# Kernel tuning notes

Hardware: AMD Instinct MI355X
Metric: run time of the kernel (lower is better)

The kernel has to match this reference:

```python
import jax, jax.numpy as jnp
import numpy as np

N_NODES = 50000
N_EDGES = 400000
N_GRAPHS = 512
F = 32        # num_features
NB = 32       # mp_num_basis_fn
ZMAX = 118
CUTOFF = 5.0
NSPH = 9      # (mp_max_degree+1)^2 with max_degree=2
DEG_IDX = jnp.array([0, 1, 1, 1, 2, 2, 2, 2, 2])  # degree of each spherical component


def _bernstein(u, n=NB):
    # reciprocal_bernstein radial basis: Bernstein polynomials of degree n-1 at u in [0,1)
    k = jnp.arange(n, dtype=jnp.float32)
    log_binom = (jax.scipy.special.gammaln(float(n)) - jax.scipy.special.gammaln(k + 1.0)
                 - jax.scipy.special.gammaln(float(n) - k))
    u = jnp.clip(u, 1e-7, 1.0 - 1e-7)[..., None]
    return jnp.exp(log_binom + k * jnp.log(u) + (float(n) - 1.0 - k) * jnp.log1p(-u))


def _smooth_cutoff(r, cutoff=CUTOFF):
    t = r / cutoff
    return jnp.where(t < 1.0, jnp.exp(1.0 - 1.0 / jnp.clip(1.0 - t * t, 1e-7, None)), 0.0)


def _sph(u):
    # real spherical harmonics (cartesian normalization) up to degree 2; u: (E,3) unit vectors
    x, y, z = u[:, 0], u[:, 1], u[:, 2]
    c = jnp.sqrt(jnp.float32(3.0))
    return jnp.stack([jnp.ones_like(x), y, z, x,
                      c * x * y, c * y * z, 0.5 * (3.0 * z * z - 1.0),
                      c * z * x, 0.5 * c * (x * x - y * y)], axis=-1)


def _dense(x, W, b):
    # equivariant Dense: shared kernel over spherical components, bias only on scalar (l=0)
    y = jnp.einsum('nmf,fg->nmg', x, W)
    return y.at[:, 0, :].add(b)


def _silu_gate(x):
    # equivariant silu: scalar channel gates all degrees (scalar part -> exact silu)
    return x * jax.nn.sigmoid(x[:, 0:1, :])


def setup_inputs() -> dict:
    key = jax.random.key(0)
    ks = jax.random.split(key, 24)
    s = 1.0 / np.sqrt(F)
    sb = 1.0 / np.sqrt(NB)
    inp = {
        'positions': 2.0 * jax.random.normal(ks[0], (N_NODES, 3), jnp.float32),
        'embed': jax.random.normal(ks[1], (ZMAX, F), jnp.float32),
        'Wy0': sb * jax.random.normal(ks[2], (3, NB, F), jnp.float32),
        'Wx0': sb * jax.random.normal(ks[3], (3, NB, F), jnp.float32),
        'W1_0': s * jax.random.normal(ks[4], (F, F), jnp.float32),
        'b1_0': jnp.zeros((F,), jnp.float32),
        'W2_0': s * jax.random.normal(ks[5], (F, F), jnp.float32),
        'b2_0': jnp.zeros((F,), jnp.float32),
        'c0': jnp.full((1,), 0.5, jnp.float32),
        'Wr_last': sb * jax.random.normal(ks[6], (NB, F), jnp.float32),
        'W1_1': s * jax.random.normal(ks[7], (F, F), jnp.float32),
        'b1_1': jnp.zeros((F,), jnp.float32),
        'W2_1': s * jax.random.normal(ks[8], (F, F), jnp.float32),
        'b2_1': jnp.zeros((F,), jnp.float32),
        'c1': jnp.full((1,), 0.5, jnp.float32),
        'Wro1': s * jax.random.normal(ks[9], (F, F), jnp.float32),
        'bro1': jnp.zeros((F,), jnp.float32),
        'Wro2': s * jax.random.normal(ks[10], (F, 1), jnp.float32),
        'bro2': jnp.zeros((1,), jnp.float32),
        'atomic_bias': jax.random.normal(ks[11], (ZMAX,), jnp.float32),
        'atomic_numbers': jax.random.randint(ks[12], (N_NODES,), 0, ZMAX, jnp.int32),
        'dst_idx': jax.random.randint(ks[13], (N_EDGES,), 0, N_NODES, jnp.int32),
        'src_idx': jax.random.randint(ks[14], (N_EDGES,), 0, N_NODES, jnp.int32),
        'batch_segments': jnp.sort(jax.random.randint(ks[15], (N_NODES,), 0, N_GRAPHS, jnp.int32)),
        'graph_mask': jnp.ones((N_GRAPHS,), jnp.bool_),
    }
    return inp


def reference(positions, embed, Wy0, Wx0, W1_0, b1_0, W2_0, b2_0, c0,
              Wr_last, W1_1, b1_1, W2_1, b2_1, c1,
              Wro1, bro1, Wro2, bro2, atomic_bias,
              atomic_numbers, dst_idx, src_idx, batch_segments, graph_mask):
    # --- edge geometry (gather_src/gather_dst) ---
    disp = positions[src_idx] - positions[dst_idx]                # (E,3)
    r = jnp.sqrt(jnp.sum(disp * disp, axis=-1) + 1e-12)           # (E,)
    u = disp / r[:, None]
    Y = _sph(u)                                                   # (E,9)
    rbf = _bernstein(r / (r + 1.0)) * _smooth_cutoff(r)[:, None]  # (E,NB)

    # --- atomic embedding, lifted to (N, 9, F) with zero higher degrees ---
    x0 = embed[atomic_numbers]                                    # (N,F)
    x = jnp.concatenate([x0[:, None, :], jnp.zeros((N_NODES, NSPH - 1, F), x0.dtype)], axis=1)

    # --- iteration 0: full-degree equivariant message pass ---
    wy = jnp.einsum('eb,lbf->elf', rbf, Wy0)[:, DEG_IDX, :]       # (E,9,F) radial weights, (0,l)->l path
    wx = jnp.einsum('eb,lbf->elf', rbf, Wx0)[:, DEG_IDX, :]       # (l,0)->l path
    xs = x[src_idx]                                               # (E,9,F)
    msg = wy * Y[:, :, None] * xs[:, 0:1, :] + wx * xs
    y = jax.ops.segment_sum(msg, dst_idx, num_segments=N_NODES)   # (N,9,F)
    y = x + y
    y = _silu_gate(_dense(y, W1_0, b1_0))
    y = _dense(y, W2_0, b2_0)
    x = x + jax.nn.silu(c0) * y                                   # y_nl == 0 (era disabled)

    # --- iteration 1 (last): max_degree=0 message pass, then reduce to scalars ---
    w0 = rbf @ Wr_last                                            # (E,F)
    msg0 = w0 * x[src_idx, 0, :]
    y0 = jax.ops.segment_sum(msg0, dst_idx, num_segments=N_NODES) # (N,F)
    xs0 = x[:, 0, :]                                              # change_max_degree -> scalars
    y0 = xs0 + y0
    y0 = jax.nn.silu(y0 @ W1_1 + b1_1)
    y0 = y0 @ W2_1 + b2_1
    xs0 = xs0 + jax.nn.silu(c1) * y0

    # --- atomic readout and per-graph sum ---
    h = jax.nn.silu(xs0 @ Wro1 + bro1)
    e_atom = (h @ Wro2)[:, 0] + bro2[0] + atomic_bias[atomic_numbers]
    e_graph = jax.ops.segment_sum(e_atom, batch_segments, num_segments=N_GRAPHS)
    return jnp.where(graph_mask, e_graph, 0.0)
```

## Files before the change

kernel.cpp:

```cpp
#include <hip/hip_runtime.h>
#include <math.h>

#define NNODES 50000
#define NEDGES 400000
#define NGRAPHS 512
#define FDIM 32
#define CAP 32

#define NHALVES 4096
#define NQ   (NNODES / NHALVES)
#define NREM (NNODES % NHALVES)

static constexpr float BINOM31[32] = {
    1.f, 31.f, 465.f, 4495.f, 31465.f, 169911.f, 736281.f, 2629575.f,
    7888725.f, 20160075.f, 44352165.f, 84672315.f, 141120525.f, 206253075.f,
    265182525.f, 300540195.f, 300540195.f, 265182525.f, 206253075.f,
    141120525.f, 84672315.f, 44352165.f, 20160075.f, 7888725.f, 2629575.f,
    736281.f, 169911.f, 31465.f, 4495.f, 465.f, 31.f, 1.f
};

__device__ __forceinline__ float fast_rcp(float x) {
    return __builtin_amdgcn_rcpf(x);
}
__device__ __forceinline__ float silu(float x) {
    return x * fast_rcp(1.0f + __expf(-x));
}

__global__ __launch_bounds__(256) void build_csr(
    const float* __restrict__ pos,
    const int* __restrict__ srci, const int* __restrict__ dsti,
    const int* __restrict__ Z,
    float4* __restrict__ pay, int* __restrict__ deg)
{
    int e = blockIdx.x * 256 + threadIdx.x;
    if (e >= NEDGES) return;
    int s = srci[e], d = dsti[e];
    float dx = pos[3 * s]     - pos[3 * d];
    float dy = pos[3 * s + 1] - pos[3 * d + 1];
    float dz = pos[3 * s + 2] - pos[3 * d + 2];
    float r = sqrtf(dx * dx + dy * dy + dz * dz + 1e-12f);
    if (r >= 5.0f) return;

    float t = r * 0.2f;
    float q = fmaxf(1.0f - t * t, 1e-7f);
    float cut = __expf(1.0f - fast_rcp(q));
    float v = fast_rcp(r + 1.0f);
    float v2 = v * v, v4 = v2 * v2, v8 = v4 * v4, v16 = v8 * v8;
    float scale = v16 * v8 * v4 * v2 * v * cut;

    int rank = atomicAdd(&deg[d], 1);
    if (rank < CAP)
        pay[(size_t)d * CAP + rank] =
            make_float4(r, scale,
                        __int_as_float(s * FDIM),
                        __int_as_float(Z[s] * FDIM));
}

#define GATHER8(ACC, XSRC, SEL)                                            \
    float ACC = 0.0f;                                                      \
    for (int j = 0; j < dgc; j += 8) {                                     \
        float rr[8], sc[8], xg[8], hh[8];                                  \
        _Pragma("unroll")                                                  \
        for (int k = 0; k < 8; ++k) {                                      \
            float4 _p = pl[j + k];                                         \
            rr[k] = _p.x; sc[k] = _p.y;                                    \
            xg[k] = (XSRC)[__float_as_int(_p.SEL) + f];                    \
        }                                                                  \
        _Pragma("unroll")                                                  \
        for (int k = 0; k < 8; ++k) hh[k] = cw[31];                        \
        _Pragma("unroll")                                                  \
        for (int t = 30; t >= 0; --t) {                                    \
            _Pragma("unroll")                                              \
            for (int k = 0; k < 8; ++k)                                    \
                hh[k] = fmaf(hh[k], rr[k], cw[t]);                         \
        }                                                                  \
        _Pragma("unroll")                                                  \
        for (int k = 0; k < 8; ++k)                                        \
            ACC = fmaf(sc[k] * hh[k], xg[k], ACC);                         \
    }

#define MATVEC32R(RES, WR, BIAS) do {                                      \
    float4 _q0=yp[0], _q1=yp[1], _q2=yp[2], _q3=yp[3];                     \
    float4 _q4=yp[4], _q5=yp[5], _q6=yp[6], _q7=yp[7];                     \
    float _a0=(BIAS), _a1=0.f, _a2=0.f, _a3=0.f;                           \
    _a0=fmaf(_q0.x,WR[ 0],_a0); _a0=fmaf(_q0.y,WR[ 1],_a0);                \
    _a0=fmaf(_q0.z,WR[ 2],_a0); _a0=fmaf(_q0.w,WR[ 3],_a0);                \
    _a1=fmaf(_q1.x,WR[ 4],_a1); _a1=fmaf(_q1.y,WR[ 5],_a1);                \
    _a1=fmaf(_q1.z,WR[ 6],_a1); _a1=fmaf(_q1.w,WR[ 7],_a1);                \
    _a2=fmaf(_q2.x,WR[ 8],_a2); _a2=fmaf(_q2.y,WR[ 9],_a2);                \
    _a2=fmaf(_q2.z,WR[10],_a2); _a2=fmaf(_q2.w,WR[11],_a2);                \
    _a3=fmaf(_q3.x,WR[12],_a3); _a3=fmaf(_q3.y,WR[13],_a3);                \
    _a3=fmaf(_q3.z,WR[14],_a3); _a3=fmaf(_q3.w,WR[15],_a3);                \
    _a0=fmaf(_q4.x,WR[16],_a0); _a0=fmaf(_q4.y,WR[17],_a0);                \
    _a0=fmaf(_q4.z,WR[18],_a0); _a0=fmaf(_q4.w,WR[19],_a0);                \
    _a1=fmaf(_q5.x,WR[20],_a1); _a1=fmaf(_q5.y,WR[21],_a1);                \
    _a1=fmaf(_q5.z,WR[22],_a1); _a1=fmaf(_q5.w,WR[23],_a1);                \
    _a2=fmaf(_q6.x,WR[24],_a2); _a2=fmaf(_q6.y,WR[25],_a2);                \
    _a2=fmaf(_q6.z,WR[26],_a2); _a2=fmaf(_q6.w,WR[27],_a2);                \
    _a3=fmaf(_q7.x,WR[28],_a3); _a3=fmaf(_q7.y,WR[29],_a3);                \
    _a3=fmaf(_q7.z,WR[30],_a3); _a3=fmaf(_q7.w,WR[31],_a3);                \
    RES = (_a0+_a1)+(_a2+_a3); } while (0)

__device__ __forceinline__ void half_range(int h, int& n0, int& n1) {
    int a = h < NREM ? h * (NQ + 1) : NREM * (NQ + 1) + (h - NREM) * NQ;
    n0 = a;
    n1 = a + (h < NREM ? NQ + 1 : NQ);
}

__global__ __launch_bounds__(256, 2) void fused_a(
    const float4* __restrict__ pay, const int* __restrict__ deg,
    const float* __restrict__ embed, const int* __restrict__ Z,
    const float* __restrict__ Wy0, const float* __restrict__ Wx0,
    const float* __restrict__ W1, const float* __restrict__ b1,
    const float* __restrict__ W2, const float* __restrict__ b2,
    const float* __restrict__ c0,
    float* __restrict__ x1buf)
{
    __shared__ __align__(16) float ylds[4][64];
    __shared__ __align__(16) float4 plds[4][2][CAP];
    int tid = threadIdx.x;
    int widx = tid >> 6;
    int lane = tid & 63;
    int f    = lane & 31;
    int half = lane >> 5;

    float cw[32], w1r[32], w2r[32];
    #pragma unroll
    for (int k = 0; k < 32; ++k) {
        cw[k]  = BINOM31[k] * (Wy0[k * FDIM + f] + Wx0[k * FDIM + f]);
        w1r[k] = W1[k * FDIM + f];
        w2r[k] = W2[k * FDIM + f];
    }
    float b1f = b1[f], b2f = b2[f];
    float sc0 = silu(c0[0]);

    int hidx = (blockIdx.x * 4 + widx) * 2 + half;
    int n0, n1;
    half_range(hidx, n0, n1);

    float* yrow = &ylds[widx][half * 32];
    const float4* yp = (const float4*)yrow;
    float4* pl = &plds[widx][half][0];

    int dgc = min(deg[n0], CAP);
    float4 pv0 = make_float4(0.f, 0.f, 0.f, 0.f);
    if (f < dgc) pv0 = pay[(size_t)n0 * CAP + f];
    int zc = Z[n0];
    pl[f] = pv0;
    float x0 = embed[zc * FDIM + f];

    for (int n = n0; n < n1; ++n) {
        int nn = (n + 1 < n1) ? n + 1 : n;
        int dgn = min(deg[nn], CAP);
        int zn  = Z[nn];
        float4 pvn = make_float4(0.f, 0.f, 0.f, 0.f);
        if (f < dgn) pvn = pay[(size_t)nn * CAP + f];

        GATHER8(accv, embed, w)

        float x0n = embed[zn * FDIM + f];
        pl[f] = pvn;

        yrow[f] = x0 + accv;
        float t;
        MATVEC32R(t, w1r, b1f);
        t = silu(t);
        yrow[f] = t;
        float u;
        MATVEC32R(u, w2r, b2f);
        x1buf[(size_t)n * FDIM + f] = fmaf(sc0, u, x0);

        dgc = dgn; x0 = x0n; zc = zn;
    }
}

__global__ __launch_bounds__(256, 2) void fused_b(
    const float4* __restrict__ pay, const int* __restrict__ deg,
    const float* __restrict__ x1buf, const float* __restrict__ Wr_last,
    const float* __restrict__ W1, const float* __restrict__ b1,
    const float* __restrict__ W2, const float* __restrict__ b2,
    const float* __restrict__ c1,
    const float* __restrict__ Wro1, const float* __restrict__ bro1,
    const float* __restrict__ Wro2, const float* __restrict__ bro2,
    const float* __restrict__ abias, const int* __restrict__ Z,
    const int* __restrict__ segs,
    float* __restrict__ out)
{
    __shared__ __align__(16) float ylds[4][64];
    __shared__ __align__(16) float4 plds[4][2][CAP];
    int tid = threadIdx.x;
    int widx = tid >> 6;
    int lane = tid & 63;
    int f    = lane & 31;
    int half = lane >> 5;

    float cw[32], w1r[32], w2r[32], wrr[32];
    #pragma unroll
    for (int k = 0; k < 32; ++k) {
        cw[k]  = BINOM31[k] * Wr_last[k * FDIM + f];
        w1r[k] = W1[k * FDIM + f];
        w2r[k] = W2[k * FDIM + f];
        wrr[k] = Wro1[k * FDIM + f];
    }
    float b1f = b1[f], b2f = b2[f], bro1f = bro1[f], wro2f = Wro2[f];
    float sc1 = silu(c1[0]);
    float bro2v = bro2[0];

    int hidx = (blockIdx.x * 4 + widx) * 2 + half;
    int n0, n1;
    half_range(hidx, n0, n1);

    float* yrow = &ylds[widx][half * 32];
    const float4* yp = (const float4*)yrow;
    float4* pl = &plds[widx][half][0];

    int dgc = min(deg[n0], CAP);
    float4 pv0 = make_float4(0.f, 0.f, 0.f, 0.f);
    if (f < dgc) pv0 = pay[(size_t)n0 * CAP + f];
    int zc = Z[n0];
    int sg = segs[n0];
    pl[f] = pv0;
    float x1 = x1buf[(size_t)n0 * FDIM + f];
    float ab = abias[zc];

    float segacc = 0.0f;
    int   curseg = -1;

    for (int n = n0; n < n1; ++n) {
        int nn = (n + 1 < n1) ? n + 1 : n;
        int dgn = min(deg[nn], CAP);
        int zn  = Z[nn];
        int sgn = segs[nn];
        float4 pvn = make_float4(0.f, 0.f, 0.f, 0.f);
        if (f < dgn) pvn = pay[(size_t)nn * CAP + f];

        GATHER8(accv, x1buf, z)

        float x1n = x1buf[(size_t)nn * FDIM + f];
        float abn = abias[zn];
        pl[f] = pvn;

        yrow[f] = x1 + accv;
        float t;
        MATVEC32R(t, w1r, b1f);
        t = silu(t);
        yrow[f] = t;
        float u;
        MATVEC32R(u, w2r, b2f);
        float xs0 = fmaf(sc1, u, x1);
        yrow[f] = xs0;
        float h;
        MATVEC32R(h, wrr, bro1f);
        float p = silu(h) * wro2f;
        p += __shfl_xor(p, 16, 32);
        p += __shfl_xor(p, 8, 32);
        p += __shfl_xor(p, 4, 32);
        p += __shfl_xor(p, 2, 32);
        p += __shfl_xor(p, 1, 32);

        if (f == 0) {
            float e = p + bro2v + ab;
            if (sg == curseg) segacc += e;
            else {
                if (curseg >= 0) atomicAdd(&out[curseg], segacc);
                curseg = sg; segacc = e;
            }
        }

        dgc = dgn; x1 = x1n; ab = abn; sg = sgn; zc = zn;
    }
    if (f == 0 && curseg >= 0) atomicAdd(&out[curseg], segacc);
}

extern "C" void kernel_launch(void* const* d_in, const int* in_sizes, int n_in,
                              void* d_out, int out_size, void* d_ws, size_t ws_size,
                              hipStream_t stream)
{
    const float* pos     = (const float*)d_in[0];
    const float* embed   = (const float*)d_in[1];
    const float* Wy0     = (const float*)d_in[2];
    const float* Wx0     = (const float*)d_in[3];
    const float* W1_0    = (const float*)d_in[4];
    const float* b1_0    = (const float*)d_in[5];
    const float* W2_0    = (const float*)d_in[6];
    const float* b2_0    = (const float*)d_in[7];
    const float* c0      = (const float*)d_in[8];
    const float* Wr_last = (const float*)d_in[9];
    const float* W1_1    = (const float*)d_in[10];
    const float* b1_1    = (const float*)d_in[11];
    const float* W2_1    = (const float*)d_in[12];
    const float* b2_1    = (const float*)d_in[13];
    const float* c1      = (const float*)d_in[14];
    const float* Wro1    = (const float*)d_in[15];
    const float* bro1    = (const float*)d_in[16];
    const float* Wro2    = (const float*)d_in[17];
    const float* bro2    = (const float*)d_in[18];
    const float* abias   = (const float*)d_in[19];
    const int*   Z       = (const int*)d_in[20];
    const int*   dsti    = (const int*)d_in[21];
    const int*   srci    = (const int*)d_in[22];
    const int*   segs    = (const int*)d_in[23];

    float* out = (float*)d_out;

    char* w = (char*)d_ws;
    float4* pay   = (float4*)w;  w += (size_t)NNODES * CAP * 16;
    float*  x1buf = (float*)w;   w += (size_t)NNODES * FDIM * 4;
    int*    deg   = (int*)w;     w += (size_t)NNODES * 4;

    const int edgeBlocks = (NEDGES + 255) / 256;
    const int persBlocks = NHALVES / 8;

    hipMemsetAsync(deg, 0, (size_t)NNODES * 4, stream);
    hipMemsetAsync(out, 0, (size_t)NGRAPHS * 4, stream);

    build_csr<<<edgeBlocks, 256, 0, stream>>>(pos, srci, dsti, Z, pay, deg);
    fused_a<<<persBlocks, 256, 0, stream>>>(pay, deg, embed, Z, Wy0, Wx0,
                                            W1_0, b1_0, W2_0, b2_0, c0, x1buf);
    fused_b<<<persBlocks, 256, 0, stream>>>(pay, deg, x1buf, Wr_last,
                                            W1_1, b1_1, W2_1, b2_1, c1,
                                            Wro1, bro1, Wro2, bro2,
                                            abias, Z, segs, out);
}
```

Before: 181.1 us.

## Process one node per full wave, splitting edges across half-waves

The fused persistent kernels now give each 64-lane wave one node at a time instead of running two independent half-waves on separate nodes. Each half handles four of every eight edges, and the two halves are combined with a cross-half shuffle. The 32x32 matvecs broadcast activations with readlane instead of writing to and reading back from shared memory. The edge payload is double-buffered in LDS, and wave-uniform degrees use readfirstlane. The aim is to shorten per-node latency and remove the LDS round trips, at the cost of twice as many sequential nodes per wave and redundant matvec work on the upper 32 lanes.

New measurement: 219.3 us. 1.21x slower.

```diff
diff --git a/kernel.cpp b/kernel.cpp
--- a/kernel.cpp
+++ b/kernel.cpp
@@ -7,9 +7,9 @@
 #define FDIM 32
 #define CAP 32
 
-#define NHALVES 4096
-#define NQ   (NNODES / NHALVES)
-#define NREM (NNODES % NHALVES)
+#define NWAVES 2048
+#define NQW   (NNODES / NWAVES)
+#define REMW  (NNODES % NWAVES)
 
 static constexpr float BINOM31[32] = {
     1.f, 31.f, 465.f, 4495.f, 31465.f, 169911.f, 736281.f, 2629575.f,
@@ -24,6 +24,9 @@
 }
 __device__ __forceinline__ float silu(float x) {
     return x * fast_rcp(1.0f + __expf(-x));
+}
+__device__ __forceinline__ float bcast(float v, int k) {
+    return __int_as_float(__builtin_amdgcn_readlane(__float_as_int(v), k));
 }
 
 __global__ __launch_bounds__(256) void build_csr(
@@ -56,55 +59,46 @@
                         __int_as_float(Z[s] * FDIM));
 }
 
-#define GATHER8(ACC, XSRC, SEL)                                            \
+#define GATHERW(ACC, XSRC, SEL)                                            \
     float ACC = 0.0f;                                                      \
     for (int j = 0; j < dgc; j += 8) {                                     \
-        float rr[8], sc[8], xg[8], hh[8];                                  \
-        _Pragma("unroll")                                                  \
-        for (int k = 0; k < 8; ++k) {                                      \
-            float4 _p = pl[j + k];                                         \
-            rr[k] = _p.x; sc[k] = _p.y;                                    \
-            xg[k] = (XSRC)[__float_as_int(_p.SEL) + f];                    \
-        }                                                                  \
-        _Pragma("unroll")                                                  \
-        for (int k = 0; k < 8; ++k) hh[k] = cw[31];                        \
+        int jb = j + (g << 2);                                             \
+        float4 q0 = plc[jb], q1 = plc[jb + 1];                             \
+        float4 q2 = plc[jb + 2], q3 = plc[jb + 3];                         \
+        float x0g = (XSRC)[__float_as_int(q0.SEL) + f];                    \
+        float x1g = (XSRC)[__float_as_int(q1.SEL) + f];                    \
+        float x2g = (XSRC)[__float_as_int(q2.SEL) + f];                    \
+        float x3g = (XSRC)[__float_as_int(q3.SEL) + f];                    \
+        float h0 = cw[31], h1 = cw[31], h2 = cw[31], h3 = cw[31];          \
         _Pragma("unroll")                                                  \
         for (int t = 30; t >= 0; --t) {                                    \
-            _Pragma("unroll")                                              \
-            for (int k = 0; k < 8; ++k)                                    \
-                hh[k] = fmaf(hh[k], rr[k], cw[t]);                         \
+            h0 = fmaf(h0, q0.x, cw[t]);                                    \
+            h1 = fmaf(h1, q1.x, cw[t]);                                    \
+            h2 = fmaf(h2, q2.x, cw[t]);                                    \
+            h3 = fmaf(h3, q3.x, cw[t]);                                    \
         }                                                                  \
-        _Pragma("unroll")                                                  \
-        for (int k = 0; k < 8; ++k)                                        \
-            ACC = fmaf(sc[k] * hh[k], xg[k], ACC);                         \
-    }
-
-#define MATVEC32R(RES, WR, BIAS) do {                                      \
-    float4 _q0=yp[0], _q1=yp[1], _q2=yp[2], _q3=yp[3];                     \
-    float4 _q4=yp[4], _q5=yp[5], _q6=yp[6], _q7=yp[7];                     \
-    float _a0=(BIAS), _a1=0.f, _a2=0.f, _a3=0.f;                           \
-    _a0=fmaf(_q0.x,WR[ 0],_a0); _a0=fmaf(_q0.y,WR[ 1],_a0);                \
-    _a0=fmaf(_q0.z,WR[ 2],_a0); _a0=fmaf(_q0.w,WR[ 3],_a0);                \
-    _a1=fmaf(_q1.x,WR[ 4],_a1); _a1=fmaf(_q1.y,WR[ 5],_a1);                \
-    _a1=fmaf(_q1.z,WR[ 6],_a1); _a1=fmaf(_q1.w,WR[ 7],_a1);                \
-    _a2=fmaf(_q2.x,WR[ 8],_a2); _a2=fmaf(_q2.y,WR[ 9],_a2);                \
-    _a2=fmaf(_q2.z,WR[10],_a2); _a2=fmaf(_q2.w,WR[11],_a2);                \
-    _a3=fmaf(_q3.x,WR[12],_a3); _a3=fmaf(_q3.y,WR[13],_a3);                \
-    _a3=fmaf(_q3.z,WR[14],_a3); _a3=fmaf(_q3.w,WR[15],_a3);                \
-    _a0=fmaf(_q4.x,WR[16],_a0); _a0=fmaf(_q4.y,WR[17],_a0);                \
-    _a0=fmaf(_q4.z,WR[18],_a0); _a0=fmaf(_q4.w,WR[19],_a0);                \
-    _a1=fmaf(_q5.x,WR[20],_a1); _a1=fmaf(_q5.y,WR[21],_a1);                \
-    _a1=fmaf(_q5.z,WR[22],_a1); _a1=fmaf(_q5.w,WR[23],_a1);                \
-    _a2=fmaf(_q6.x,WR[24],_a2); _a2=fmaf(_q6.y,WR[25],_a2);                \
-    _a2=fmaf(_q6.z,WR[26],_a2); _a2=fmaf(_q6.w,WR[27],_a2);                \
-    _a3=fmaf(_q7.x,WR[28],_a3); _a3=fmaf(_q7.y,WR[29],_a3);                \
-    _a3=fmaf(_q7.z,WR[30],_a3); _a3=fmaf(_q7.w,WR[31],_a3);                \
-    RES = (_a0+_a1)+(_a2+_a3); } while (0)
-
-__device__ __forceinline__ void half_range(int h, int& n0, int& n1) {
-    int a = h < NREM ? h * (NQ + 1) : NREM * (NQ + 1) + (h - NREM) * NQ;
+        ACC = fmaf(q0.y * h0, x0g, ACC);                                   \
+        ACC = fmaf(q1.y * h1, x1g, ACC);                                   \
+        ACC = fmaf(q2.y * h2, x2g, ACC);                                   \
+        ACC = fmaf(q3.y * h3, x3g, ACC);                                   \
+    }                                                                      \
+    ACC += __shfl_xor(ACC, 32);
+
+#define MATVECW(RES, WR, BIAS, YSRC) do {                                  \
+    float _a0 = (BIAS), _a1 = 0.f, _a2 = 0.f, _a3 = 0.f;                   \
+    _Pragma("unroll")                                                      \
+    for (int k = 0; k < 32; k += 4) {                                      \
+        _a0 = fmaf(bcast((YSRC), k    ), WR[k    ], _a0);                  \
+        _a1 = fmaf(bcast((YSRC), k + 1), WR[k + 1], _a1);                  \
+        _a2 = fmaf(bcast((YSRC), k + 2), WR[k + 2], _a2);                  \
+        _a3 = fmaf(bcast((YSRC), k + 3), WR[k + 3], _a3);                  \
+    }                                                                      \
+    RES = (_a0 + _a1) + (_a2 + _a3); } while (0)
+
+__device__ __forceinline__ void wave_range(int h, int& n0, int& n1) {
+    int a = h < REMW ? h * (NQW + 1) : REMW * (NQW + 1) + (h - REMW) * NQW;
     n0 = a;
-    n1 = a + (h < NREM ? NQ + 1 : NQ);
+    n1 = a + (h < REMW ? NQW + 1 : NQW);
 }
 
 __global__ __launch_bounds__(256, 2) void fused_a(
@@ -116,13 +110,12 @@
     const float* __restrict__ c0,
     float* __restrict__ x1buf)
 {
-    __shared__ __align__(16) float ylds[4][64];
     __shared__ __align__(16) float4 plds[4][2][CAP];
     int tid = threadIdx.x;
     int widx = tid >> 6;
     int lane = tid & 63;
     int f    = lane & 31;
-    int half = lane >> 5;
+    int g    = lane >> 5;
 
     float cw[32], w1r[32], w2r[32];
     #pragma unroll
@@ -134,43 +127,43 @@
     float b1f = b1[f], b2f = b2[f];
     float sc0 = silu(c0[0]);
 
-    int hidx = (blockIdx.x * 4 + widx) * 2 + half;
+    int wid = blockIdx.x * 4 + widx;
     int n0, n1;
-    half_range(hidx, n0, n1);
-
-    float* yrow = &ylds[widx][half * 32];
-    const float4* yp = (const float4*)yrow;
-    float4* pl = &plds[widx][half][0];
-
-    int dgc = min(deg[n0], CAP);
+    wave_range(wid, n0, n1);
+
+    const float4* plc = &plds[widx][0][0];
+    float4*       pln = &plds[widx][1][0];
+
+    int dg0 = min(deg[n0], CAP);
     float4 pv0 = make_float4(0.f, 0.f, 0.f, 0.f);
-    if (f < dgc) pv0 = pay[(size_t)n0 * CAP + f];
-    int zc = Z[n0];
-    pl[f] = pv0;
-    float x0 = embed[zc * FDIM + f];
+    if (lane < dg0) pv0 = pay[(size_t)n0 * CAP + lane];
+    if (lane < 32) ((float4*)plc)[lane] = pv0;
+    int dgc = __builtin_amdgcn_readfirstlane(dg0);
+    float x0 = embed[Z[n0] * FDIM + f];
 
     for (int n = n0; n < n1; ++n) {
         int nn = (n + 1 < n1) ? n + 1 : n;
         int dgn = min(deg[nn], CAP);
-        int zn  = Z[nn];
         float4 pvn = make_float4(0.f, 0.f, 0.f, 0.f);
-        if (f < dgn) pvn = pay[(size_t)nn * CAP + f];
-
-        GATHER8(accv, embed, w)
-
-        float x0n = embed[zn * FDIM + f];
-        pl[f] = pvn;
-
-        yrow[f] = x0 + accv;
+        if (lane < dgn) pvn = pay[(size_t)nn * CAP + lane];
+        float x0n = embed[Z[nn] * FDIM + f];
+
+        GATHERW(accv, embed, w)
+
+        if (lane < 32) pln[lane] = pvn;
+
+        float yv = x0 + accv;
         float t;
-        MATVEC32R(t, w1r, b1f);
+        MATVECW(t, w1r, b1f, yv);
         t = silu(t);
-        yrow[f] = t;
         float u;
-        MATVEC32R(u, w2r, b2f);
-        x1buf[(size_t)n * FDIM + f] = fmaf(sc0, u, x0);
-
-        dgc = dgn; x0 = x0n; zc = zn;
+        MATVECW(u, w2r, b2f, t);
+        if (lane < 32)
+            x1buf[(size_t)n * FDIM + f] = fmaf(sc0, u, x0);
+
+        const float4* tp = plc; plc = (const float4*)pln; pln = (float4*)tp;
+        dgc = __builtin_amdgcn_readfirstlane(dgn);
+        x0 = x0n;
     }
 }
 
@@ -186,13 +179,12 @@
     const int* __restrict__ segs,
     float* __restrict__ out)
 {
-    __shared__ __align__(16) float ylds[4][64];
     __shared__ __align__(16) float4 plds[4][2][CAP];
     int tid = threadIdx.x;
     int widx = tid >> 6;
     int lane = tid & 63;
     int f    = lane & 31;
-    int half = lane >> 5;
+    int g    = lane >> 5;
 
     float cw[32], w1r[32], w2r[32], wrr[32];
     #pragma unroll
@@ -206,22 +198,21 @@
     float sc1 = silu(c1[0]);
     float bro2v = bro2[0];
 
-    int hidx = (blockIdx.x * 4 + widx) * 2 + half;
+    int wid = blockIdx.x * 4 + widx;
     int n0, n1;
-    half_range(hidx, n0, n1);
-
-    float* yrow = &ylds[widx][half * 32];
-    const float4* yp = (const float4*)yrow;
-    float4* pl = &plds[widx][half][0];
-
-    int dgc = min(deg[n0], CAP);
+    wave_range(wid, n0, n1);
+
+    const float4* plc = &plds[widx][0][0];
+    float4*       pln = &plds[widx][1][0];
+
+    int dg0 = min(deg[n0], CAP);
     float4 pv0 = make_float4(0.f, 0.f, 0.f, 0.f);
-    if (f < dgc) pv0 = pay[(size_t)n0 * CAP + f];
-    int zc = Z[n0];
-    int sg = segs[n0];
-    pl[f] = pv0;
+    if (lane < dg0) pv0 = pay[(size_t)n0 * CAP + lane];
+    if (lane < 32) ((float4*)plc)[lane] = pv0;
+    int dgc = __builtin_amdgcn_readfirstlane(dg0);
     float x1 = x1buf[(size_t)n0 * FDIM + f];
-    float ab = abias[zc];
+    float ab = abias[Z[n0]];
+    int   sg = segs[n0];
 
     float segacc = 0.0f;
     int   curseg = -1;
@@ -229,28 +220,25 @@
     for (int n = n0; n < n1; ++n) {
         int nn = (n + 1 < n1) ? n + 1 : n;
         int dgn = min(deg[nn], CAP);
-        int zn  = Z[nn];
-        int sgn = segs[nn];
         float4 pvn = make_float4(0.f, 0.f, 0.f, 0.f);
-        if (f < dgn) pvn = pay[(size_t)nn * CAP + f];
-
-        GATHER8(accv, x1buf, z)
-
+        if (lane < dgn) pvn = pay[(size_t)nn * CAP + lane];
         float x1n = x1buf[(size_t)nn * FDIM + f];
-        float abn = abias[zn];
-        pl[f] = pvn;
-
-        yrow[f] = x1 + accv;
+        float abn = abias[Z[nn]];
+        int   sgn = segs[nn];
+
+        GATHERW(accv, x1buf, z)
+
+        if (lane < 32) pln[lane] = pvn;
+
+        float yv = x1 + accv;
         float t;
-        MATVEC32R(t, w1r, b1f);
+        MATVECW(t, w1r, b1f, yv);
         t = silu(t);
-        yrow[f] = t;
         float u;
-        MATVEC32R(u, w2r, b2f);
+        MATVECW(u, w2r, b2f, t);
         float xs0 = fmaf(sc1, u, x1);
-        yrow[f] = xs0;
         float h;
-        MATVEC32R(h, wrr, bro1f);
+        MATVECW(h, wrr, bro1f, xs0);
         float p = silu(h) * wro2f;
         p += __shfl_xor(p, 16, 32);
         p += __shfl_xor(p, 8, 32);
@@ -258,7 +246,7 @@
         p += __shfl_xor(p, 2, 32);
         p += __shfl_xor(p, 1, 32);
 
-        if (f == 0) {
+        if (lane == 0) {
             float e = p + bro2v + ab;
             if (sg == curseg) segacc += e;
             else {
@@ -267,9 +255,11 @@
             }
         }
 
-        dgc = dgn; x1 = x1n; ab = abn; sg = sgn; zc = zn;
+        const float4* tp = plc; plc = (const float4*)pln; pln = (float4*)tp;
+        dgc = __builtin_amdgcn_readfirstlane(dgn);
+        x1 = x1n; ab = abn; sg = sgn;
     }
-    if (f == 0 && curseg >= 0) atomicAdd(&out[curseg], segacc);
+    if (lane == 0 && curseg >= 0) atomicAdd(&out[curseg], segacc);
 }
 
 extern "C" void kernel_launch(void* const* d_in, const int* in_sizes, int n_in,
@@ -309,7 +299,7 @@
     int*    deg   = (int*)w;     w += (size_t)NNODES * 4;
 
     const int edgeBlocks = (NEDGES + 255) / 256;
-    const int persBlocks = NHALVES / 8;
+    const int persBlocks = NWAVES / 4;
 
     hipMemsetAsync(deg, 0, (size_t)NNODES * 4, stream);
     hipMemsetAsync(out, 0, (size_t)NGRAPHS * 4, stream);
```
